# Performance work log

Hardware: AMD Instinct MI355X
Metric: run time of the kernel (lower is better)

The kernel has to match this reference:

```python
import jax, jax.numpy as jnp
import numpy as np

B, N_HIST, N_PRED = 32, 12, 12
N_NODE, INPUT_DIM, OUTPUT_DIM = 325, 2, 1
HIDDEN, N_RNN_LAYERS = 256, 2
EDGE_DIM, NODE_DIM, ORDER = 2, 64, 2
K = ORDER * EDGE_DIM + 1  # number of concat blocks per GraphConv


def setup_inputs() -> dict:
    key = jax.random.key(0)
    ks = iter(jax.random.split(key, 40))

    def rn(shape, s=0.05):
        return jax.random.normal(next(ks), shape, jnp.float32) * s

    L, H = N_RNN_LAYERS, HIDDEN
    d = {}
    d['inputs'] = jax.random.normal(next(ks), (B, N_HIST, N_NODE, INPUT_DIM), jnp.float32)
    d['vertexes'] = rn((N_NODE, NODE_DIM), 1.0)
    d['arcs_w0'] = rn((2 * NODE_DIM, 4 * NODE_DIM)); d['arcs_b0'] = jnp.zeros((4 * NODE_DIM,), jnp.float32)
    d['arcs_w1'] = rn((4 * NODE_DIM, 4 * NODE_DIM)); d['arcs_b1'] = jnp.zeros((4 * NODE_DIM,), jnp.float32)
    d['arcs_w2'] = rn((4 * NODE_DIM, EDGE_DIM)); d['arcs_b2'] = jnp.zeros((EDGE_DIM,), jnp.float32)
    d['enc_pre_w0'] = rn((K * INPUT_DIM, H)); d['enc_pre_b0'] = jnp.zeros((H,), jnp.float32)
    d['enc_pre_w1'] = rn((K * H, H)); d['enc_pre_b1'] = jnp.zeros((H,), jnp.float32)
    d['enc_wih'] = rn((L, 4 * H, H)); d['enc_whh'] = rn((L, 4 * H, H))
    d['enc_bih'] = jnp.zeros((L, 4 * H), jnp.float32); d['enc_bhh'] = jnp.zeros((L, 4 * H), jnp.float32)
    d['dec_pre_w0'] = rn((K * OUTPUT_DIM, H)); d['dec_pre_b0'] = jnp.zeros((H,), jnp.float32)
    d['dec_pre_w1'] = rn((K * H, H)); d['dec_pre_b1'] = jnp.zeros((H,), jnp.float32)
    d['dec_wih'] = rn((L, 4 * H, H)); d['dec_whh'] = rn((L, 4 * H, H))
    d['dec_bih'] = jnp.zeros((L, 4 * H), jnp.float32); d['dec_bhh'] = jnp.zeros((L, 4 * H), jnp.float32)
    d['dec_post_w0'] = rn((K * H, H)); d['dec_post_b0'] = jnp.zeros((H,), jnp.float32)
    d['dec_post_w1'] = rn((K * H, H)); d['dec_post_b1'] = jnp.zeros((H,), jnp.float32)
    d['proj_w'] = rn((H, OUTPUT_DIM)); d['proj_b'] = jnp.zeros((OUTPUT_DIM,), jnp.float32)
    return d


def _graph_conv(x, supports, w, b):
    out = [x]
    for e in range(supports.shape[0]):
        a = supports[e]
        x1 = x
        for _ in range(ORDER):
            x1 = jnp.einsum('...vc,vw->...wc', x1, a)
            out.append(x1)
    return jnp.concatenate(out, -1) @ w + b


def _stacked_gc(x, supports, layers):
    for w, b in layers:
        x = jax.nn.relu(_graph_conv(x, supports, w, b))
    return x


def _lstm_step(x, h, c, wih, whh, bih, bhh):
    # x: [BN, H]; h, c: [L, BN, H]; torch gate order i, f, g, o
    new_h, new_c = [], []
    for l in range(N_RNN_LAYERS):
        gates = x @ wih[l].T + bih[l] + h[l] @ whh[l].T + bhh[l]
        i, f, g, o = jnp.split(gates, 4, axis=-1)
        cn = jax.nn.sigmoid(f) * c[l] + jax.nn.sigmoid(i) * jnp.tanh(g)
        hn = jax.nn.sigmoid(o) * jnp.tanh(cn)
        new_h.append(hn); new_c.append(cn)
        x = hn
    return x, jnp.stack(new_h), jnp.stack(new_c)


def _adaptive_supports(vertexes, arcs_w0, arcs_b0, arcs_w1, arcs_b1, arcs_w2, arcs_b2):
    n = vertexes.shape[0]
    src = jnp.broadcast_to(vertexes[None, :, :], (n, n, NODE_DIM))
    dst = jnp.broadcast_to(vertexes[:, None, :], (n, n, NODE_DIM))
    h = jnp.concatenate([src, dst], -1)
    h = jax.nn.leaky_relu(h @ arcs_w0 + arcs_b0)
    h = jax.nn.leaky_relu(h @ arcs_w1 + arcs_b1)
    adj = jnp.transpose(h @ arcs_w2 + arcs_b2, (2, 0, 1))  # [E, N, N]
    adj = jax.nn.relu(adj)
    adj = adj / jnp.maximum(jnp.sum(jnp.abs(adj), axis=2, keepdims=True), 1e-12)
    # FAITHFUL to source: adj is computed but the function returns identity.expand(adj.shape)
    return jnp.broadcast_to(jnp.eye(n, dtype=jnp.float32)[None], adj.shape)


def _forward(inputs, vertexes, arcs_w0, arcs_b0, arcs_w1, arcs_b1, arcs_w2, arcs_b2,
             enc_pre_w0, enc_pre_b0, enc_pre_w1, enc_pre_b1,
             enc_wih, enc_whh, enc_bih, enc_bhh,
             dec_pre_w0, dec_pre_b0, dec_pre_w1, dec_pre_b1,
             dec_wih, dec_whh, dec_bih, dec_bhh,
             dec_post_w0, dec_post_b0, dec_post_w1, dec_post_b1,
             proj_w, proj_b):
    b, t, n, _ = inputs.shape
    H, L = HIDDEN, N_RNN_LAYERS
    supports = _adaptive_supports(vertexes, arcs_w0, arcs_b0, arcs_w1, arcs_b1, arcs_w2, arcs_b2)

    # ---- encoding ----
    x = _stacked_gc(inputs, supports, [(enc_pre_w0, enc_pre_b0), (enc_pre_w1, enc_pre_b1)])  # [B,T,N,H]
    seq = jnp.transpose(x, (1, 0, 2, 3)).reshape(t, b * n, H)
    h0 = jnp.zeros((L, b * n, H), inputs.dtype)
    c0 = jnp.zeros((L, b * n, H), inputs.dtype)

    def enc_step(carry, xt):
        hh, cc = carry
        _, hh, cc = _lstm_step(xt, hh, cc, enc_wih, enc_whh, enc_bih, enc_bhh)
        return (hh, cc), None

    (h, c), _ = jax.lax.scan(enc_step, (h0, c0), seq)
    # NOTE: source calls torch.dropout but discards the result -> no-op; reproduced by omission.

    dec_in0 = jnp.zeros((b, n, OUTPUT_DIM), inputs.dtype)
    dec_pre = [(dec_pre_w0, dec_pre_b0), (dec_pre_w1, dec_pre_b1)]
    dec_post = [(dec_post_w0, dec_post_b0), (dec_post_w1, dec_post_b1)]

    def dec_step(carry, _):
        x, hh, cc = carry
        x = _stacked_gc(x, supports, dec_pre)                      # [B,N,H]
        xf, hh, cc = _lstm_step(x.reshape(b * n, H), hh, cc, dec_wih, dec_whh, dec_bih, dec_bhh)
        x = _stacked_gc(xf.reshape(b, n, H), supports, dec_post)   # [B,N,H]
        out = x @ proj_w + proj_b                                  # [B,N,out_dim]
        return (out, hh, cc), out

    _, outs = jax.lax.scan(dec_step, (dec_in0, h, c), None, length=N_PRED)
    return jnp.transpose(outs, (1, 0, 2, 3))  # [B, n_pred, N, output_dim]


def reference(inputs, vertexes, arcs_w0, arcs_b0, arcs_w1, arcs_b1, arcs_w2, arcs_b2,
              enc_pre_w0, enc_pre_b0, enc_pre_w1, enc_pre_b1,
              enc_wih, enc_whh, enc_bih, enc_bhh,
              dec_pre_w0, dec_pre_b0, dec_pre_w1, dec_pre_b1,
              dec_wih, dec_whh, dec_bih, dec_bhh,
              dec_post_w0, dec_post_b0, dec_post_w1, dec_post_b1,
              proj_w, proj_b):
    return _forward(inputs, vertexes, arcs_w0, arcs_b0, arcs_w1, arcs_b1, arcs_w2, arcs_b2,
                    enc_pre_w0, enc_pre_b0, enc_pre_w1, enc_pre_b1,
                    enc_wih, enc_whh, enc_bih, enc_bhh,
                    dec_pre_w0, dec_pre_b0, dec_pre_w1, dec_pre_b1,
                    dec_wih, dec_whh, dec_bih, dec_bhh,
                    dec_post_w0, dec_post_b0, dec_post_w1, dec_post_b1,
                    proj_w, proj_b)
```

## Files before the change

### kernel.cpp

```cpp
#include <hip/hip_runtime.h>
#include <math.h>

#define BATCH 32
#define NNODE 325
#define T_HIST 12
#define T_PRED 12
#define H 256
#define G4 1024
#define ROWS (BATCH*NNODE)
#define MPAD 10496

typedef __attribute__((ext_vector_type(8))) short bf16x8;
typedef __attribute__((ext_vector_type(4))) float f32x4;
typedef unsigned short ushort_t;
typedef unsigned int uint_t;

#define GLL16(gp, sp) __builtin_amdgcn_global_load_lds( \
    (const __attribute__((address_space(1))) void*)(gp), \
    (__attribute__((address_space(3))) void*)(sp), 16, 0, 0)

__device__ inline float bf2f(ushort_t u) { return __uint_as_float(((uint_t)u) << 16); }

__device__ inline void split2(float v, ushort_t& h, ushort_t& l) {
    uint_t b = __float_as_uint(v);
    uint_t hb = (b + 0x7fffu + ((b >> 16) & 1u)) & 0xffff0000u;
    h = (ushort_t)(hb >> 16);
    float r = v - __uint_as_float(hb);
    uint_t rb = __float_as_uint(r);
    l = (ushort_t)((rb + 0x7fffu + ((rb >> 16) & 1u)) >> 16);
}

__device__ inline float sigm(float x) {
    x = fminf(fmaxf(x, -30.f), 30.f);
    return 1.f / (1.f + __expf(-x));
}
__device__ inline float tanh_f(float x) {
    x = fminf(fmaxf(x, -15.f), 15.f);
    float e = __expf(2.f * x);
    return (e - 1.f) / (e + 1.f);
}

__global__ void collapse_kernel(const float* __restrict__ w, float* __restrict__ out,
                                int cin, int nblk) {
    int idx = blockIdx.x * blockDim.x + threadIdx.x;
    if (idx >= cin * H) return;
    int c = idx / H, h = idx % H;
    float s = 0.f;
    for (int k = 0; k < nblk; ++k) s += w[(size_t)(k * cin + c) * H + h];
    out[idx] = s;
}

__global__ void pack_big_kernel(const float* __restrict__ wih, const float* __restrict__ whh,
                                const float* __restrict__ bih, const float* __restrict__ bhh,
                                ushort_t* __restrict__ Bxh, ushort_t* __restrict__ Bxl,
                                ushort_t* __restrict__ Bhh, ushort_t* __restrict__ Bhl,
                                float* __restrict__ biasI) {
    int idx = blockIdx.x * blockDim.x + threadIdx.x;
    if (idx >= 32 * G4) return;
    int kg = idx >> 10, col = idx & 1023;
    int j = col >> 2, g = col & 3;
    int gcol = g * 256 + j;
    if (kg == 0) biasI[col] = bih[gcol] + bhh[gcol];
#pragma unroll
    for (int jj = 0; jj < 8; ++jj) {
        int k = kg * 8 + jj;
        ushort_t hh, ll;
        split2(wih[(size_t)gcol * H + k], hh, ll);
        Bxh[(size_t)idx * 8 + jj] = hh; Bxl[(size_t)idx * 8 + jj] = ll;
        split2(whh[(size_t)gcol * H + k], hh, ll);
        Bhh[(size_t)idx * 8 + jj] = hh; Bhl[(size_t)idx * 8 + jj] = ll;
    }
}

__global__ void pack_small_kernel(const float* __restrict__ w,
                                  ushort_t* __restrict__ Bh, ushort_t* __restrict__ Bl) {
    int idx = blockIdx.x * blockDim.x + threadIdx.x;
    if (idx >= 32 * H) return;
    int kg = idx >> 8, n = idx & 255;
#pragma unroll
    for (int jj = 0; jj < 8; ++jj) {
        int k = kg * 8 + jj;
        float s = 0.f;
        for (int blk = 0; blk < 5; ++blk) s += w[(size_t)(blk * H + k) * H + n];
        ushort_t hh, ll; split2(s, hh, ll);
        Bh[(size_t)idx * 8 + jj] = hh; Bl[(size_t)idx * 8 + jj] = ll;
    }
}

__global__ void enc_pre0_pk(const float* __restrict__ inp, const float* __restrict__ w,
                            const float* __restrict__ b, ushort_t* __restrict__ oh,
                            ushort_t* __restrict__ ol, int t) {
    int m = blockIdx.x * 256 + threadIdx.x;
    int kg = blockIdx.y;
    float ip0 = 0.f, ip1 = 0.f;
    if (m < ROWS) {
        int bb = m / NNODE, nn = m % NNODE;
        const float* ip = inp + (((size_t)bb * T_HIST + t) * NNODE + nn) * 2;
        ip0 = ip[0]; ip1 = ip[1];
    }
    union { ushort_t u[8]; bf16x8 v; } hc, lc;
#pragma unroll
    for (int jj = 0; jj < 8; ++jj) {
        int j = kg * 8 + jj;
        float v = (m < ROWS) ? fmaxf(ip0 * w[j] + ip1 * w[H + j] + b[j], 0.f) : 0.f;
        split2(v, hc.u[jj], lc.u[jj]);
    }
    size_t base = ((size_t)kg * MPAD + m) * 8;
    *(bf16x8*)&oh[base] = hc.v;
    *(bf16x8*)&ol[base] = lc.v;
}

__global__ void dec_pre0_pk(const float* __restrict__ y, const float* __restrict__ w,
                            const float* __restrict__ b, ushort_t* __restrict__ oh,
                            ushort_t* __restrict__ ol) {
    int m = blockIdx.x * 256 + threadIdx.x;
    int kg = blockIdx.y;
    float yv = y[m];
    union { ushort_t u[8]; bf16x8 v; } hc, lc;
#pragma unroll
    for (int jj = 0; jj < 8; ++jj) {
        int j = kg * 8 + jj;
        float v = fmaxf(yv * w[j] + b[j], 0.f);
        split2(v, hc.u[jj], lc.u[jj]);
    }
    size_t base = ((size_t)kg * MPAD + m) * 8;
    *(bf16x8*)&oh[base] = hc.v;
    *(bf16x8*)&ol[base] = lc.v;
}

template<bool GATES, int NSC, int HSC, int BNT, int NBG, int MINW>
__global__ __launch_bounds__(256, MINW) void gemm_k(
    const ushort_t* __restrict__ AxH, const ushort_t* __restrict__ AxL,
    const ushort_t* __restrict__ AhH, const ushort_t* __restrict__ AhL,
    const ushort_t* __restrict__ BxH, const ushort_t* __restrict__ BxL,
    const ushort_t* __restrict__ BhH, const ushort_t* __restrict__ BhL,
    const float* __restrict__ bias, float* __restrict__ cst,
    ushort_t* __restrict__ OH, ushort_t* __restrict__ OL,
    int nbx, int doSwz)
{
    constexpr int BCH = BNT * 4;
    constexpr int JB  = BNT / 32;
    __shared__ __align__(16) ushort_t As[2][2][4096];
    __shared__ __align__(16) ushort_t Bs[2][2][BCH * 8];

    int bid = blockIdx.x;
    if (doSwz) { int cpx = gridDim.x >> 3; bid = (bid & 7) * cpx + (bid >> 3); }
    const int bm = (bid / nbx) * 128, bn = (bid % nbx) * BNT;
    const int tid = threadIdx.x, lane = tid & 63;
    const int wm = (tid >> 7) & 1, wn = (tid >> 6) & 1;
    const int l15 = lane & 15, lk = lane >> 4;

    auto stageSC = [&](int s, int slot) {
        const ushort_t *Ah, *Al, *Bh, *Bl; int ck;
        if (s < HSC) { Ah = AxH; Al = AxL; Bh = BxH; Bl = BxL; ck = s; }
        else         { Ah = AhH; Al = AhL; Bh = BhH; Bl = BhL; ck = s - HSC; }
#pragma unroll
        for (int q = 0; q < 2; ++q) {
            int ubase = (tid & 192) + q * 256;
            int u = ubase + lane;
            int kgl = u >> 7, rc = u & 127;
            size_t ga = ((size_t)(ck * 4 + kgl) * MPAD + bm + rc) * 8;
            GLL16(Ah + ga, &As[slot][0][ubase * 8]);
            GLL16(Al + ga, &As[slot][1][ubase * 8]);
        }
        {
            int ubase = tid & 192;
            int u = tid;
            int kgl = u >> 6, nc = u & 63;
            size_t gb = ((size_t)(ck * 4 + kgl) * NBG + bn + nc) * 8;
            GLL16(Bh + gb, &Bs[slot][0][ubase * 8]);
            GLL16(Bl + gb, &Bs[slot][1][ubase * 8]);
        }
    };

    f32x4 acc[4][JB] = {};

    stageSC(0, 0);

#pragma unroll
    for (int s = 0; s < NSC; ++s) {
        __builtin_amdgcn_s_barrier();
        if (s + 1 < NSC) {
            stageSC(s + 1, (s + 1) & 1);
            asm volatile("s_waitcnt vmcnt(6)" ::: "memory");
        } else {
            asm volatile("s_waitcnt vmcnt(0)" ::: "memory");
        }
        __builtin_amdgcn_s_barrier();
        __builtin_amdgcn_sched_barrier(0);

        const int slot = s & 1;
        bf16x8 ah[4], al[4], bh[JB], bl[JB];
#pragma unroll
        for (int i = 0; i < 4; ++i) {
            int ea = (lk * 128 + wm * 64 + i * 16 + l15) * 8;
            ah[i] = *(const bf16x8*)&As[slot][0][ea];
            al[i] = *(const bf16x8*)&As[slot][1][ea];
        }
#pragma unroll
        for (int j = 0; j < JB; ++j) {
            int eb = (lk * BNT + wn * (BNT / 2) + j * 16 + l15) * 8;
            bh[j] = *(const bf16x8*)&Bs[slot][0][eb];
            bl[j] = *(const bf16x8*)&Bs[slot][1][eb];
        }
#pragma unroll
        for (int i = 0; i < 4; ++i)
#pragma unroll
            for (int j = 0; j < JB; ++j)
                acc[i][j] = __builtin_amdgcn_mfma_f32_16x16x32_bf16(bh[j], ah[i], acc[i][j], 0, 0, 0);
#pragma unroll
        for (int i = 0; i < 4; ++i)
#pragma unroll
            for (int j = 0; j < JB; ++j)
                acc[i][j] = __builtin_amdgcn_mfma_f32_16x16x32_bf16(bl[j], ah[i], acc[i][j], 0, 0, 0);
#pragma unroll
        for (int i = 0; i < 4; ++i)
#pragma unroll
            for (int j = 0; j < JB; ++j)
                acc[i][j] = __builtin_amdgcn_mfma_f32_16x16x32_bf16(bh[j], al[i], acc[i][j], 0, 0, 0);
    }

    if constexpr (GATES) {
        uint_t* Hs = (uint_t*)&As[0][0][0];
        const int jb0 = (bn >> 2) + wn * 8;
#pragma unroll
        for (int j = 0; j < JB; ++j) {
            float4 b4 = *(const float4*)&bias[bn + wn * 32 + j * 16 + lk * 4];
            int cell = jb0 + j * 4 + lk;
#pragma unroll
            for (int i = 0; i < 4; ++i) {
                int m = bm + wm * 64 + i * 16 + l15;
                float vi = acc[i][j][0] + b4.x;
                float vf = acc[i][j][1] + b4.y;
                float vg = acc[i][j][2] + b4.z;
                float vo = acc[i][j][3] + b4.w;
                size_t ci = (size_t)cell * MPAD + m;
                float cold = cst[ci];
                float cn = sigm(vf) * cold + sigm(vi) * tanh_f(vg);
                float hn = sigm(vo) * tanh_f(cn);
                cst[ci] = cn;
                ushort_t hh, hl; split2(hn, hh, hl);
                Hs[(wm * 64 + i * 16 + l15) * 17 + wn * 8 + j * 4 + lk] = ((uint_t)hh << 16) | hl;
            }
        }
        __syncthreads();
        {
            int mloc = tid & 127, kgl = tid >> 7;
            union { ushort_t u[8]; bf16x8 v; } hi, lo;
#pragma unroll
            for (int jj = 0; jj < 8; ++jj) {
                uint_t wv = Hs[mloc * 17 + kgl * 8 + jj];
                hi.u[jj] = (ushort_t)(wv >> 16);
                lo.u[jj] = (ushort_t)(wv & 0xffffu);
            }
            size_t base = ((size_t)((bn >> 5) + kgl) * MPAD + bm + mloc) * 8;
            *(bf16x8*)&OH[base] = hi.v;
            *(bf16x8*)&OL[base] = lo.v;
        }
    } else {
#pragma unroll
        for (int j = 0; j < JB; ++j) {
            float4 b4 = *(const float4*)&bias[bn + wn * (BNT / 2) + j * 16 + lk * 4];
#pragma unroll
            for (int i = 0; i < 4; ++i) {
                float v0 = fmaxf(acc[i][j][0] + b4.x, 0.f);
                float v1 = fmaxf(acc[i][j][1] + b4.y, 0.f);
                float v2 = fmaxf(acc[i][j][2] + b4.z, 0.f);
                float v3 = fmaxf(acc[i][j][3] + b4.w, 0.f);
                ushort_t h0, h1, h2, h3, l0, l1, l2, l3;
                split2(v0, h0, l0); split2(v1, h1, l1);
                split2(v2, h2, l2); split2(v3, h3, l3);
                uint_t hu0 = (uint_t)h0 | ((uint_t)h1 << 16), hu1 = (uint_t)h2 | ((uint_t)h3 << 16);
                uint_t lu0 = (uint_t)l0 | ((uint_t)l1 << 16), lu1 = (uint_t)l2 | ((uint_t)l3 << 16);
                uint_t ph0 = (uint_t)__shfl_xor((int)hu0, 16, 64);
                uint_t ph1 = (uint_t)__shfl_xor((int)hu1, 16, 64);
                uint_t pl0 = (uint_t)__shfl_xor((int)lu0, 16, 64);
                uint_t pl1 = (uint_t)__shfl_xor((int)lu1, 16, 64);
                int kgg = ((bn + wn * (BNT / 2) + j * 16) >> 3) + (lk >> 1);
                size_t base = ((size_t)kgg * MPAD + bm + wm * 64 + i * 16 + l15) * 8;
                union { uint_t u2[4]; bf16x8 v; } ch;
                if ((lk & 1) == 0) {
                    ch.u2[0] = hu0; ch.u2[1] = hu1; ch.u2[2] = ph0; ch.u2[3] = ph1;
                    *(bf16x8*)&OH[base] = ch.v;
                } else {
                    ch.u2[0] = pl0; ch.u2[1] = pl1; ch.u2[2] = lu0; ch.u2[3] = lu1;
                    *(bf16x8*)&OL[base] = ch.v;
                }
            }
        }
    }
}

__global__ void proj_kernel(const ushort_t* __restrict__ xh, const ushort_t* __restrict__ xl,
                            const float* __restrict__ pw, const float* __restrict__ pb,
                            float* __restrict__ y, float* __restrict__ out, int t) {
    int wid = threadIdx.x >> 6, lane = threadIdx.x & 63;
    int r = blockIdx.x * 4 + wid;
    if (r >= ROWS) return;
    const int kg = lane >> 1, sub = (lane & 1) * 4;
    size_t base = ((size_t)kg * MPAD + r) * 8 + sub;
    float s = 0.f;
#pragma unroll
    for (int q = 0; q < 4; ++q) {
        int k = kg * 8 + sub + q;
        s += (bf2f(xh[base + q]) + bf2f(xl[base + q])) * pw[k];
    }
#pragma unroll
    for (int off = 32; off > 0; off >>= 1) s += __shfl_down(s, off, 64);
    if (lane == 0) {
        float v = s + pb[0];
        y[r] = v;
        int bb = r / NNODE, n = r % NNODE;
        out[((size_t)bb * T_PRED + t) * NNODE + n] = v;
    }
}

static inline void gemm_big(const ushort_t* xH, const ushort_t* xL,
                            const ushort_t* hH, const ushort_t* hL,
                            ushort_t* const* B, const float* bias, float* c,
                            ushort_t* oH, ushort_t* oL, hipStream_t s) {
    gemm_k<true, 16, 8, 64, 1024, 3><<<82 * 16, 256, 0, s>>>(
        xH, xL, hH, hL, B[0], B[1], B[2], B[3], bias, c, oH, oL, 16, 1);
}
static inline void gemm_small(const ushort_t* aH, const ushort_t* aL,
                              const ushort_t* bH, const ushort_t* bL, const float* bias,
                              ushort_t* oH, ushort_t* oL, hipStream_t s) {
    gemm_k<false, 8, 8, 64, 256, 3><<<82 * 4, 256, 0, s>>>(
        aH, aL, aH, aL, bH, bL, bH, bL, bias, nullptr, oH, oL, 4, 1);
}

extern "C" void kernel_launch(void* const* d_in, const int* in_sizes, int n_in,
                              void* d_out, int out_size, void* d_ws, size_t ws_size,
                              hipStream_t stream) {
    (void)in_sizes; (void)n_in; (void)out_size; (void)ws_size;

    const float* inputs      = (const float*)d_in[0];
    const float* enc_pre_w0  = (const float*)d_in[8];
    const float* enc_pre_b0  = (const float*)d_in[9];
    const float* enc_pre_w1  = (const float*)d_in[10];
    const float* enc_pre_b1  = (const float*)d_in[11];
    const float* enc_wih     = (const float*)d_in[12];
    const float* enc_whh     = (const float*)d_in[13];
    const float* enc_bih     = (const float*)d_in[14];
    const float* enc_bhh     = (const float*)d_in[15];
    const float* dec_pre_w0  = (const float*)d_in[16];
    const float* dec_pre_b0  = (const float*)d_in[17];
    const float* dec_pre_w1  = (const float*)d_in[18];
    const float* dec_pre_b1  = (const float*)d_in[19];
    const float* dec_wih     = (const float*)d_in[20];
    const float* dec_whh     = (const float*)d_in[21];
    const float* dec_bih     = (const float*)d_in[22];
    const float* dec_bhh     = (const float*)d_in[23];
    const float* dec_post_w0 = (const float*)d_in[24];
    const float* dec_post_b0 = (const float*)d_in[25];
    const float* dec_post_w1 = (const float*)d_in[26];
    const float* dec_post_b1 = (const float*)d_in[27];
    const float* proj_w      = (const float*)d_in[28];
    const float* proj_b      = (const float*)d_in[29];
    float* out = (float*)d_out;

    char* wsb = (char*)d_ws;
    size_t off = 0;
    auto allocF = [&](size_t n) { float* p = (float*)(wsb + off); off += ((n * 4 + 15) & ~(size_t)15); return p; };
    auto allocU = [&](size_t n) { ushort_t* p = (ushort_t*)(wsb + off); off += ((n * 2 + 15) & ~(size_t)15); return p; };

    const size_t BIGW = (size_t)32 * G4 * 8;
    const size_t SMLW = (size_t)32 * H * 8;
    const size_t ACT  = (size_t)32 * MPAD * 8;

    ushort_t* eB0[4]; ushort_t* eB1[4]; ushort_t* dB0[4]; ushort_t* dB1[4];
    for (int q = 0; q < 4; ++q) eB0[q] = allocU(BIGW);
    for (int q = 0; q < 4; ++q) eB1[q] = allocU(BIGW);
    for (int q = 0; q < 4; ++q) dB0[q] = allocU(BIGW);
    for (int q = 0; q < 4; ++q) dB1[q] = allocU(BIGW);
    float* eBI0 = allocF(G4); float* eBI1 = allocF(G4);
    float* dBI0 = allocF(G4); float* dBI1 = allocF(G4);
    ushort_t* eP1h = allocU(SMLW); ushort_t* eP1l = allocU(SMLW);
    ushort_t* dP1h = allocU(SMLW); ushort_t* dP1l = allocU(SMLW);
    ushort_t* po0h = allocU(SMLW); ushort_t* po0l = allocU(SMLW);
    ushort_t* po1h = allocU(SMLW); ushort_t* po1l = allocU(SMLW);
    float* encW0eff = allocF(2 * H);
    float* decPre0eff = allocF(H);
    ushort_t* h0H[2]; ushort_t* h0L[2]; ushort_t* h1H[2]; ushort_t* h1L[2];
    for (int q = 0; q < 2; ++q) { h0H[q] = allocU(ACT); h0L[q] = allocU(ACT); }
    for (int q = 0; q < 2; ++q) { h1H[q] = allocU(ACT); h1L[q] = allocU(ACT); }
    float* c0 = allocF((size_t)H * MPAD);
    float* c1 = allocF((size_t)H * MPAD);
    ushort_t* xaH = allocU(ACT); ushort_t* xaL = allocU(ACT);
    ushort_t* xbH = allocU(ACT); ushort_t* xbL = allocU(ACT);
    float* y = allocF(MPAD);

    const size_t LOFF = (size_t)G4 * H;
    const int EW = 256;

    pack_big_kernel<<<128, EW, 0, stream>>>(enc_wih, enc_whh, enc_bih, enc_bhh,
                                            eB0[0], eB0[1], eB0[2], eB0[3], eBI0);
    pack_big_kernel<<<128, EW, 0, stream>>>(enc_wih + LOFF, enc_whh + LOFF, enc_bih + G4, enc_bhh + G4,
                                            eB1[0], eB1[1], eB1[2], eB1[3], eBI1);
    pack_big_kernel<<<128, EW, 0, stream>>>(dec_wih, dec_whh, dec_bih, dec_bhh,
                                            dB0[0], dB0[1], dB0[2], dB0[3], dBI0);
    pack_big_kernel<<<128, EW, 0, stream>>>(dec_wih + LOFF, dec_whh + LOFF, dec_bih + G4, dec_bhh + G4,
                                            dB1[0], dB1[1], dB1[2], dB1[3], dBI1);
    pack_small_kernel<<<32, EW, 0, stream>>>(enc_pre_w1, eP1h, eP1l);
    pack_small_kernel<<<32, EW, 0, stream>>>(dec_pre_w1, dP1h, dP1l);
    pack_small_kernel<<<32, EW, 0, stream>>>(dec_post_w0, po0h, po0l);
    pack_small_kernel<<<32, EW, 0, stream>>>(dec_post_w1, po1h, po1l);
    collapse_kernel<<<2, EW, 0, stream>>>(enc_pre_w0, encW0eff, 2, 5);
    collapse_kernel<<<1, EW, 0, stream>>>(dec_pre_w0, decPre0eff, 1, 5);

    for (int q = 0; q < 2; ++q) {
        hipMemsetAsync(h0H[q], 0, ACT * 2, stream); hipMemsetAsync(h0L[q], 0, ACT * 2, stream);
        hipMemsetAsync(h1H[q], 0, ACT * 2, stream); hipMemsetAsync(h1L[q], 0, ACT * 2, stream);
    }
    hipMemsetAsync(c0, 0, (size_t)H * MPAD * 4, stream);
    hipMemsetAsync(c1, 0, (size_t)H * MPAD * 4, stream);
    hipMemsetAsync(y, 0, (size_t)MPAD * 4, stream);

    const dim3 PG(MPAD / 256, 32);

    for (int t = 0; t < T_HIST; ++t) {
        int pr = t & 1;
        enc_pre0_pk<<<PG, EW, 0, stream>>>(inputs, encW0eff, enc_pre_b0, xaH, xaL, t);
        gemm_small(xaH, xaL, eP1h, eP1l, enc_pre_b1, xbH, xbL, stream);
        gemm_big(xbH, xbL, h0H[pr], h0L[pr], eB0, eBI0, c0, h0H[pr ^ 1], h0L[pr ^ 1], stream);
        gemm_big(h0H[pr ^ 1], h0L[pr ^ 1], h1H[pr], h1L[pr], eB1, eBI1, c1, h1H[pr ^ 1], h1L[pr ^ 1], stream);
    }

    for (int d = 0; d < T_PRED; ++d) {
        int pr = d & 1;
        dec_pre0_pk<<<PG, EW, 0, stream>>>(y, decPre0eff, dec_pre_b0, xaH, xaL);
        gemm_small(xaH, xaL, dP1h, dP1l, dec_pre_b1, xbH, xbL, stream);
        gemm_big(xbH, xbL, h0H[pr], h0L[pr], dB0, dBI0, c0, h0H[pr ^ 1], h0L[pr ^ 1], stream);
        gemm_big(h0H[pr ^ 1], h0L[pr ^ 1], h1H[pr], h1L[pr], dB1, dBI1, c1, h1H[pr ^ 1], h1L[pr ^ 1], stream);
        gemm_small(h1H[pr ^ 1], h1L[pr ^ 1], po0h, po0l, dec_post_b0, xaH, xaL, stream);
        gemm_small(xaH, xaL, po1h, po1l, dec_post_b1, xbH, xbL, stream);
        proj_kernel<<<(ROWS + 3) / 4, EW, 0, stream>>>(xbH, xbL, proj_w, proj_b, y, out, d);
    }
}
```

Baseline: 2.447 ms.

## Load low-half bf16 operands straight to registers, halving LDS staging

The low-order bf16 halves of the A and B operands are now loaded from global memory directly into registers one k-step ahead, and only the high halves go through LDS. The main loop is unrolled in pairs with ping-pong register buffers. A large padding LDS array, kept alive by a dummy store, holds LDS use near its old level so occupancy stays the same, and the gates epilogue reuses it as scratch. The aim is less LDS traffic and fewer LDS reads per step, at the cost of more VGPRs and uncoalesced direct global loads, and the loop assumes NSC is even.

```diff
diff --git a/kernel.cpp b/kernel.cpp
--- a/kernel.cpp
+++ b/kernel.cpp
@@ -140,8 +140,9 @@
 {
     constexpr int BCH = BNT * 4;
     constexpr int JB  = BNT / 32;
-    __shared__ __align__(16) ushort_t As[2][2][4096];
-    __shared__ __align__(16) ushort_t Bs[2][2][BCH * 8];
+    __shared__ __align__(16) ushort_t As[2][4096];
+    __shared__ __align__(16) ushort_t Bs[2][BCH * 8];
+    __shared__ __align__(16) ushort_t ldspad[10240];
 
     int bid = blockIdx.x;
     if (doSwz) { int cpx = gridDim.x >> 3; bid = (bid & 7) * cpx + (bid >> 3); }
@@ -150,78 +151,89 @@
     const int wm = (tid >> 7) & 1, wn = (tid >> 6) & 1;
     const int l15 = lane & 15, lk = lane >> 4;
 
+    if (nbx == -12345) ldspad[tid] = (ushort_t)tid;
+
     auto stageSC = [&](int s, int slot) {
-        const ushort_t *Ah, *Al, *Bh, *Bl; int ck;
-        if (s < HSC) { Ah = AxH; Al = AxL; Bh = BxH; Bl = BxL; ck = s; }
-        else         { Ah = AhH; Al = AhL; Bh = BhH; Bl = BhL; ck = s - HSC; }
+        const ushort_t *Ah, *Bh; int ck;
+        if (s < HSC) { Ah = AxH; Bh = BxH; ck = s; }
+        else         { Ah = AhH; Bh = BhH; ck = s - HSC; }
 #pragma unroll
         for (int q = 0; q < 2; ++q) {
             int ubase = (tid & 192) + q * 256;
             int u = ubase + lane;
             int kgl = u >> 7, rc = u & 127;
             size_t ga = ((size_t)(ck * 4 + kgl) * MPAD + bm + rc) * 8;
-            GLL16(Ah + ga, &As[slot][0][ubase * 8]);
-            GLL16(Al + ga, &As[slot][1][ubase * 8]);
+            GLL16(Ah + ga, &As[slot][ubase * 8]);
         }
         {
             int ubase = tid & 192;
-            int u = tid;
-            int kgl = u >> 6, nc = u & 63;
+            int kgl = tid >> 6, nc = tid & 63;
             size_t gb = ((size_t)(ck * 4 + kgl) * NBG + bn + nc) * 8;
-            GLL16(Bh + gb, &Bs[slot][0][ubase * 8]);
-            GLL16(Bl + gb, &Bs[slot][1][ubase * 8]);
+            GLL16(Bh + gb, &Bs[slot][ubase * 8]);
         }
     };
+    auto loadRegs = [&](int s, bf16x8* alr, bf16x8* blr) {
+        const ushort_t *Al, *Bl; int ck;
+        if (s < HSC) { Al = AxL; Bl = BxL; ck = s; }
+        else         { Al = AhL; Bl = BhL; ck = s - HSC; }
+#pragma unroll
+        for (int i = 0; i < 4; ++i)
+            alr[i] = *(const bf16x8*)&Al[((size_t)(ck * 4 + lk) * MPAD + bm + wm * 64 + i * 16 + l15) * 8];
+#pragma unroll
+        for (int j = 0; j < JB; ++j)
+            blr[j] = *(const bf16x8*)&Bl[((size_t)(ck * 4 + lk) * NBG + bn + wn * (BNT / 2) + j * 16 + l15) * 8];
+    };
+
+#define K_STEP(S, SLOT, CAL, CBL, NAL, NBL) do {                               \
+        __builtin_amdgcn_s_barrier();                                          \
+        if ((S) + 1 < NSC) { stageSC((S) + 1, (SLOT) ^ 1);                     \
+                             loadRegs((S) + 1, NAL, NBL); }                    \
+        __builtin_amdgcn_sched_barrier(0);                                     \
+        if ((S) + 1 < NSC) asm volatile("s_waitcnt vmcnt(9)" ::: "memory");    \
+        else               asm volatile("s_waitcnt vmcnt(0)" ::: "memory");    \
+        __builtin_amdgcn_s_barrier();                                          \
+        __builtin_amdgcn_sched_barrier(0);                                     \
+        {                                                                      \
+            bf16x8 ah[4], bh[JB];                                              \
+            _Pragma("unroll")                                                  \
+            for (int j = 0; j < JB; ++j)                                       \
+                bh[j] = *(const bf16x8*)&Bs[SLOT][(lk * BNT + wn * (BNT / 2) + j * 16 + l15) * 8]; \
+            _Pragma("unroll")                                                  \
+            for (int i = 0; i < 4; ++i)                                        \
+                ah[i] = *(const bf16x8*)&As[SLOT][(lk * 128 + wm * 64 + i * 16 + l15) * 8]; \
+            _Pragma("unroll")                                                  \
+            for (int i = 0; i < 4; ++i)                                        \
+                _Pragma("unroll")                                              \
+                for (int j = 0; j < JB; ++j)                                   \
+                    acc[i][j] = __builtin_amdgcn_mfma_f32_16x16x32_bf16(bh[j], CAL[i], acc[i][j], 0, 0, 0); \
+            _Pragma("unroll")                                                  \
+            for (int i = 0; i < 4; ++i)                                        \
+                _Pragma("unroll")                                              \
+                for (int j = 0; j < JB; ++j)                                   \
+                    acc[i][j] = __builtin_amdgcn_mfma_f32_16x16x32_bf16(bh[j], ah[i], acc[i][j], 0, 0, 0); \
+            _Pragma("unroll")                                                  \
+            for (int i = 0; i < 4; ++i)                                        \
+                _Pragma("unroll")                                              \
+                for (int j = 0; j < JB; ++j)                                   \
+                    acc[i][j] = __builtin_amdgcn_mfma_f32_16x16x32_bf16(CBL[j], ah[i], acc[i][j], 0, 0, 0); \
+        }                                                                      \
+    } while (0)
 
     f32x4 acc[4][JB] = {};
+    bf16x8 alA[4], blA[JB], alB[4], blB[JB];
 
     stageSC(0, 0);
-
-#pragma unroll
-    for (int s = 0; s < NSC; ++s) {
-        __builtin_amdgcn_s_barrier();
-        if (s + 1 < NSC) {
-            stageSC(s + 1, (s + 1) & 1);
-            asm volatile("s_waitcnt vmcnt(6)" ::: "memory");
-        } else {
-            asm volatile("s_waitcnt vmcnt(0)" ::: "memory");
-        }
-        __builtin_amdgcn_s_barrier();
-        __builtin_amdgcn_sched_barrier(0);
-
-        const int slot = s & 1;
-        bf16x8 ah[4], al[4], bh[JB], bl[JB];
-#pragma unroll
-        for (int i = 0; i < 4; ++i) {
-            int ea = (lk * 128 + wm * 64 + i * 16 + l15) * 8;
-            ah[i] = *(const bf16x8*)&As[slot][0][ea];
-            al[i] = *(const bf16x8*)&As[slot][1][ea];
-        }
-#pragma unroll
-        for (int j = 0; j < JB; ++j) {
-            int eb = (lk * BNT + wn * (BNT / 2) + j * 16 + l15) * 8;
-            bh[j] = *(const bf16x8*)&Bs[slot][0][eb];
-            bl[j] = *(const bf16x8*)&Bs[slot][1][eb];
-        }
-#pragma unroll
-        for (int i = 0; i < 4; ++i)
-#pragma unroll
-            for (int j = 0; j < JB; ++j)
-                acc[i][j] = __builtin_amdgcn_mfma_f32_16x16x32_bf16(bh[j], ah[i], acc[i][j], 0, 0, 0);
-#pragma unroll
-        for (int i = 0; i < 4; ++i)
-#pragma unroll
-            for (int j = 0; j < JB; ++j)
-                acc[i][j] = __builtin_amdgcn_mfma_f32_16x16x32_bf16(bl[j], ah[i], acc[i][j], 0, 0, 0);
-#pragma unroll
-        for (int i = 0; i < 4; ++i)
-#pragma unroll
-            for (int j = 0; j < JB; ++j)
-                acc[i][j] = __builtin_amdgcn_mfma_f32_16x16x32_bf16(bh[j], al[i], acc[i][j], 0, 0, 0);
-    }
+    loadRegs(0, alA, blA);
+
+#pragma unroll
+    for (int sp = 0; sp < NSC / 2; ++sp) {
+        K_STEP(2 * sp,     0, alA, blA, alB, blB);
+        K_STEP(2 * sp + 1, 1, alB, blB, alA, blA);
+    }
+#undef K_STEP
 
     if constexpr (GATES) {
-        uint_t* Hs = (uint_t*)&As[0][0][0];
+        uint_t* Hs = (uint_t*)&ldspad[0];
         const int jb0 = (bn >> 2) + wn * 8;
 #pragma unroll
         for (int j = 0; j < JB; ++j) {
```

Measured after the change: 3.778 ms. +54.4%, slower.

## Wavefront-pipeline encoder LSTM layers into paired single-launch gate GEMMs

Applied to the files above, without the earlier changes.

The encoder loop is skewed so that layer 1 at step t and layer 0 at step t+1 run in one launch. A combined kernel picks its argument set by block index, which doubles the grid for these launches and halves the number of big-GEMM launches in the encoder. s_setprio is also raised around the MFMA block to favour compute waves. The main risk is the hidden-state buffer parity: layer 0 writes h0 into the buffer that layer 1 reads in the same launch, so correctness depends on which ping-pong slot each side uses.

```diff
diff --git a/kernel.cpp b/kernel.cpp
--- a/kernel.cpp
+++ b/kernel.cpp
@@ -128,23 +128,21 @@
     *(bf16x8*)&ol[base] = lc.v;
 }
 
-template<bool GATES, int NSC, int HSC, int BNT, int NBG, int MINW>
-__global__ __launch_bounds__(256, MINW) void gemm_k(
-    const ushort_t* __restrict__ AxH, const ushort_t* __restrict__ AxL,
-    const ushort_t* __restrict__ AhH, const ushort_t* __restrict__ AhL,
-    const ushort_t* __restrict__ BxH, const ushort_t* __restrict__ BxL,
-    const ushort_t* __restrict__ BhH, const ushort_t* __restrict__ BhL,
-    const float* __restrict__ bias, float* __restrict__ cst,
-    ushort_t* __restrict__ OH, ushort_t* __restrict__ OL,
-    int nbx, int doSwz)
+template<bool GATES, int NSC, int HSC, int BNT, int NBG>
+__device__ __forceinline__ void gemm_body(
+    const ushort_t* AxH, const ushort_t* AxL,
+    const ushort_t* AhH, const ushort_t* AhL,
+    const ushort_t* BxH, const ushort_t* BxL,
+    const ushort_t* BhH, const ushort_t* BhL,
+    const float* bias, float* cst,
+    ushort_t* OH, ushort_t* OL,
+    int nbx, int bid)
 {
     constexpr int BCH = BNT * 4;
     constexpr int JB  = BNT / 32;
     __shared__ __align__(16) ushort_t As[2][2][4096];
     __shared__ __align__(16) ushort_t Bs[2][2][BCH * 8];
 
-    int bid = blockIdx.x;
-    if (doSwz) { int cpx = gridDim.x >> 3; bid = (bid & 7) * cpx + (bid >> 3); }
     const int bm = (bid / nbx) * 128, bn = (bid % nbx) * BNT;
     const int tid = threadIdx.x, lane = tid & 63;
     const int wm = (tid >> 7) & 1, wn = (tid >> 6) & 1;
@@ -165,8 +163,7 @@
         }
         {
             int ubase = tid & 192;
-            int u = tid;
-            int kgl = u >> 6, nc = u & 63;
+            int kgl = tid >> 6, nc = tid & 63;
             size_t gb = ((size_t)(ck * 4 + kgl) * NBG + bn + nc) * 8;
             GLL16(Bh + gb, &Bs[slot][0][ubase * 8]);
             GLL16(Bl + gb, &Bs[slot][1][ubase * 8]);
@@ -203,6 +200,7 @@
             bh[j] = *(const bf16x8*)&Bs[slot][0][eb];
             bl[j] = *(const bf16x8*)&Bs[slot][1][eb];
         }
+        __builtin_amdgcn_s_setprio(1);
 #pragma unroll
         for (int i = 0; i < 4; ++i)
 #pragma unroll
@@ -218,6 +216,7 @@
 #pragma unroll
             for (int j = 0; j < JB; ++j)
                 acc[i][j] = __builtin_amdgcn_mfma_f32_16x16x32_bf16(bh[j], al[i], acc[i][j], 0, 0, 0);
+        __builtin_amdgcn_s_setprio(0);
     }
 
     if constexpr (GATES) {
@@ -291,6 +290,53 @@
     }
 }
 
+struct GArgs {
+    const ushort_t *AxH, *AxL, *AhH, *AhL;
+    const ushort_t *BxH, *BxL, *BhH, *BhL;
+    const float* bias;
+    float* cst;
+    ushort_t *OH, *OL;
+};
+
+template<bool GATES, int NSC, int HSC, int BNT, int NBG, int MINW>
+__global__ __launch_bounds__(256, MINW) void gemm_k(
+    const ushort_t* __restrict__ AxH, const ushort_t* __restrict__ AxL,
+    const ushort_t* __restrict__ AhH, const ushort_t* __restrict__ AhL,
+    const ushort_t* __restrict__ BxH, const ushort_t* __restrict__ BxL,
+    const ushort_t* __restrict__ BhH, const ushort_t* __restrict__ BhL,
+    const float* __restrict__ bias, float* __restrict__ cst,
+    ushort_t* __restrict__ OH, ushort_t* __restrict__ OL,
+    int nbx, int doSwz)
+{
+    int bid = blockIdx.x;
+    if (doSwz) { int cpx = gridDim.x >> 3; bid = (bid & 7) * cpx + (bid >> 3); }
+    gemm_body<GATES, NSC, HSC, BNT, NBG>(AxH, AxL, AhH, AhL, BxH, BxL, BhH, BhL,
+                                         bias, cst, OH, OL, nbx, bid);
+}
+
+__global__ __launch_bounds__(256, 3) void gemm_big_pair(GArgs a, GArgs b, int nblk0) {
+    int raw = blockIdx.x;
+    int sel = raw >= nblk0;
+    int local = sel ? raw - nblk0 : raw;
+    int cnt = sel ? (int)gridDim.x - nblk0 : nblk0;
+    int cpx = cnt >> 3;
+    int bid = (local & 7) * cpx + (local >> 3);
+    const ushort_t* AxH = sel ? b.AxH : a.AxH;
+    const ushort_t* AxL = sel ? b.AxL : a.AxL;
+    const ushort_t* AhH = sel ? b.AhH : a.AhH;
+    const ushort_t* AhL = sel ? b.AhL : a.AhL;
+    const ushort_t* BxH = sel ? b.BxH : a.BxH;
+    const ushort_t* BxL = sel ? b.BxL : a.BxL;
+    const ushort_t* BhH = sel ? b.BhH : a.BhH;
+    const ushort_t* BhL = sel ? b.BhL : a.BhL;
+    const float* bias = sel ? b.bias : a.bias;
+    float* cst = sel ? b.cst : a.cst;
+    ushort_t* OH = sel ? b.OH : a.OH;
+    ushort_t* OL = sel ? b.OL : a.OL;
+    gemm_body<true, 16, 8, 64, 1024>(AxH, AxL, AhH, AhL, BxH, BxL, BhH, BhL,
+                                     bias, cst, OH, OL, 16, bid);
+}
+
 __global__ void proj_kernel(const ushort_t* __restrict__ xh, const ushort_t* __restrict__ xl,
                             const float* __restrict__ pw, const float* __restrict__ pb,
                             float* __restrict__ y, float* __restrict__ out, int t) {
@@ -315,12 +361,21 @@
     }
 }
 
-static inline void gemm_big(const ushort_t* xH, const ushort_t* xL,
-                            const ushort_t* hH, const ushort_t* hL,
-                            ushort_t* const* B, const float* bias, float* c,
-                            ushort_t* oH, ushort_t* oL, hipStream_t s) {
-    gemm_k<true, 16, 8, 64, 1024, 3><<<82 * 16, 256, 0, s>>>(
-        xH, xL, hH, hL, B[0], B[1], B[2], B[3], bias, c, oH, oL, 16, 1);
+static inline GArgs mkargs(const ushort_t* xH, const ushort_t* xL,
+                           const ushort_t* hH, const ushort_t* hL,
+                           ushort_t* const* B, const float* bias, float* c,
+                           ushort_t* oH, ushort_t* oL) {
+    GArgs g;
+    g.AxH = xH; g.AxL = xL; g.AhH = hH; g.AhL = hL;
+    g.BxH = B[0]; g.BxL = B[1]; g.BhH = B[2]; g.BhL = B[3];
+    g.bias = bias; g.cst = c; g.OH = oH; g.OL = oL;
+    return g;
+}
+static inline void big_single(const GArgs& g, hipStream_t s) {
+    gemm_big_pair<<<1312, 256, 0, s>>>(g, g, 1312);
+}
+static inline void big_pair(const GArgs& g0, const GArgs& g1, hipStream_t s) {
+    gemm_big_pair<<<2624, 256, 0, s>>>(g0, g1, 1312);
 }
 static inline void gemm_small(const ushort_t* aH, const ushort_t* aL,
                               const ushort_t* bH, const ushort_t* bL, const float* bias,
@@ -418,20 +473,29 @@
 
     const dim3 PG(MPAD / 256, 32);
 
-    for (int t = 0; t < T_HIST; ++t) {
+    enc_pre0_pk<<<PG, EW, 0, stream>>>(inputs, encW0eff, enc_pre_b0, xaH, xaL, 0);
+    gemm_small(xaH, xaL, eP1h, eP1l, enc_pre_b1, xbH, xbL, stream);
+    big_single(mkargs(xbH, xbL, h0H[0], h0L[0], eB0, eBI0, c0, h0H[1], h0L[1]), stream);
+    for (int t = 0; t < T_HIST - 1; ++t) {
         int pr = t & 1;
-        enc_pre0_pk<<<PG, EW, 0, stream>>>(inputs, encW0eff, enc_pre_b0, xaH, xaL, t);
+        enc_pre0_pk<<<PG, EW, 0, stream>>>(inputs, encW0eff, enc_pre_b0, xaH, xaL, t + 1);
         gemm_small(xaH, xaL, eP1h, eP1l, enc_pre_b1, xbH, xbL, stream);
-        gemm_big(xbH, xbL, h0H[pr], h0L[pr], eB0, eBI0, c0, h0H[pr ^ 1], h0L[pr ^ 1], stream);
-        gemm_big(h0H[pr ^ 1], h0L[pr ^ 1], h1H[pr], h1L[pr], eB1, eBI1, c1, h1H[pr ^ 1], h1L[pr ^ 1], stream);
-    }
+        GArgs gL1 = mkargs(h0H[pr ^ 1], h0L[pr ^ 1], h1H[pr], h1L[pr],
+                           eB1, eBI1, c1, h1H[pr ^ 1], h1L[pr ^ 1]);
+        GArgs gL0 = mkargs(xbH, xbL, h0H[pr ^ 1], h0L[pr ^ 1],
+                           eB0, eBI0, c0, h0H[pr], h0L[pr]);
+        big_pair(gL1, gL0, stream);
+    }
+    big_single(mkargs(h0H[0], h0L[0], h1H[1], h1L[1], eB1, eBI1, c1, h1H[0], h1L[0]), stream);
 
     for (int d = 0; d < T_PRED; ++d) {
         int pr = d & 1;
         dec_pre0_pk<<<PG, EW, 0, stream>>>(y, decPre0eff, dec_pre_b0, xaH, xaL);
         gemm_small(xaH, xaL, dP1h, dP1l, dec_pre_b1, xbH, xbL, stream);
-        gemm_big(xbH, xbL, h0H[pr], h0L[pr], dB0, dBI0, c0, h0H[pr ^ 1], h0L[pr ^ 1], stream);
-        gemm_big(h0H[pr ^ 1], h0L[pr ^ 1], h1H[pr], h1L[pr], dB1, dBI1, c1, h1H[pr ^ 1], h1L[pr ^ 1], stream);
+        big_single(mkargs(xbH, xbL, h0H[pr], h0L[pr], dB0, dBI0, c0,
+                          h0H[pr ^ 1], h0L[pr ^ 1]), stream);
+        big_single(mkargs(h0H[pr ^ 1], h0L[pr ^ 1], h1H[pr], h1L[pr], dB1, dBI1, c1,
+                          h1H[pr ^ 1], h1L[pr ^ 1]), stream);
         gemm_small(h1H[pr ^ 1], h1L[pr ^ 1], po0h, po0l, dec_post_b0, xaH, xaL, stream);
         gemm_small(xaH, xaL, po1h, po1l, dec_post_b1, xbH, xbL, stream);
         proj_kernel<<<(ROWS + 3) / 4, EW, 0, stream>>>(xbH, xbL, proj_w, proj_b, y, out, d);
```

Result: no change. 2.473 ms (+1.1%).
